# Optimization experiments

Measured on AMD Instinct MI355X. Metric: run time of the kernel, lower is better.

Reference implementation:

```python
import jax, jax.numpy as jnp
import numpy as np

SEQ_LEN = 12  # configs['seq_len']
B, N, E = 4, 50000, 1600000
F_IN, F_OUT = 12, 48


def setup_inputs() -> dict:
    key = jax.random.key(0)
    k_x, k_ei, k_ew, k_w = jax.random.split(key, 4)
    x = jax.random.normal(k_x, (B, N, F_IN), dtype=jnp.float32)
    edge_index = jax.random.randint(k_ei, (B, 2, E), 0, N, dtype=jnp.int32)
    edge_attr = jax.random.uniform(k_ew, (B, E), dtype=jnp.float32)  # positive edge weights
    W = jax.random.normal(k_w, (F_IN, F_OUT), dtype=jnp.float32) * (1.0 / np.sqrt(F_IN))
    b = jnp.zeros((F_OUT,), dtype=jnp.float32)
    return {"x": x, "edge_index": edge_index, "edge_attr": edge_attr, "W": W, "b": b}


def _gcn_conv(x, src, dst, ew, W, b):
    # PyG GCNConv with edge_weight: A_hat = D^-1/2 (A + I) D^-1/2, x' = A_hat x W + b
    n = x.shape[0]
    xw = x @ W                                            # [N, F_OUT]
    deg = jax.ops.segment_sum(ew, dst, num_segments=n) + 1.0  # +1 for self loop weight
    dinv = jax.lax.rsqrt(deg)                             # deg > 0 guaranteed by self loops
    norm = dinv[src] * ew * dinv[dst]                     # [E]
    msg = xw[src] * norm[:, None]                         # [E, F_OUT] gathered messages
    agg = jax.ops.segment_sum(msg, dst, num_segments=n)   # scatter-add to destinations
    agg = agg + xw * (dinv * dinv)[:, None]               # self-loop contribution (weight 1)
    return agg + b


def reference(x, edge_index, edge_attr, W, b):
    def one_graph(xg, eig, ewg):
        h = _gcn_conv(xg, eig[0], eig[1], ewg, W, b)      # [N, F_OUT]
        # dropout is identity in eval mode
        h = h.reshape(h.shape[0], SEQ_LEN, -1)            # [N, seq_len, d]
        return jnp.transpose(h, (1, 0, 2))                # [seq_len, N, d]

    return jax.vmap(one_graph)(x, edge_index, edge_attr)  # stacked: [B, seq_len, N, d]
```

## Files before the change

kernel.cpp:

```cpp
#include <hip/hip_runtime.h>

#define BATCH 4
#define NNODE 50000
#define NEDGE 1600000
#define F_IN 12
#define F_OUT 48
#define SEQ 12

#define BNODE 64
#define NBUCK ((NNODE + BNODE - 1) / BNODE)
#define NBINS (BATCH * NBUCK)
#define SCAN_N 4096
#define EBLK 4096
#define EPB_C (EBLK / 256)
#define EPB_F (EBLK / 512)
#define NFB ((NEDGE + EBLK - 1) / EBLK)
#define CAPB 2560
#define MAXR (CAPB / 256)

typedef float f4v __attribute__((ext_vector_type(4)));


__global__ void __launch_bounds__(256) k_zero(int* __restrict__ cnt) {
    int i = blockIdx.x * 256 + threadIdx.x;
    if (i < SCAN_N) cnt[i] = 0;
}

__global__ void __launch_bounds__(256) k_count(const int* __restrict__ ei,
                                               int* __restrict__ cnt) {
    __shared__ int h[NBUCK];
    int t = threadIdx.x;
    for (int i = t; i < NBUCK; i += 256) h[i] = 0;
    __syncthreads();
    int b = blockIdx.y;
    int e0 = blockIdx.x * EBLK;
    const int* dsts = ei + ((size_t)b * 2 + 1) * NEDGE;
    for (int it = 0; it < EPB_C; ++it) {
        int e = e0 + it * 256 + t;
        if (e < NEDGE) atomicAdd(&h[dsts[e] >> 6], 1);
    }
    __syncthreads();
    for (int i = t; i < NBUCK; i += 256) {
        int c = h[i];
        if (c) atomicAdd(&cnt[b * NBUCK + i], c);
    }
}

__global__ void __launch_bounds__(256) k_scan(const int* __restrict__ cnt,
                                              int* __restrict__ off,
                                              int* __restrict__ cur) {
    __shared__ int w[256];
    int t = threadIdx.x;
    int base = t * 16;
    int loc[16];
    int s = 0;
#pragma unroll
    for (int j = 0; j < 16; j++) { loc[j] = cnt[base + j]; s += loc[j]; }
    w[t] = s;
    __syncthreads();
    for (int d = 1; d < 256; d <<= 1) {
        int v = (t >= d) ? w[t - d] : 0;
        __syncthreads();
        w[t] += v;
        __syncthreads();
    }
    int run = w[t] - s;
#pragma unroll
    for (int j = 0; j < 16; j++) {
        int i = base + j;
        off[i] = run;
        if (i < NBINS) cur[i] = run;
        run += loc[j];
    }
}

__global__ void __launch_bounds__(512) k_fill(const int* __restrict__ ei,
                                              const float* __restrict__ ew,
                                              int* __restrict__ cur,
                                              int2* __restrict__ rec) {
    __shared__ int h[1024];
    __shared__ int loff[1024];
    __shared__ int gbase[NBUCK];
    __shared__ int2 srec[EBLK];
    __shared__ int w[512];

    int t = threadIdx.x;
    int b = blockIdx.y;
    int e0 = blockIdx.x * EBLK;
    for (int i = t; i < 1024; i += 512) h[i] = 0;
    __syncthreads();

    const size_t ebase = (size_t)b * 2 * NEDGE;
    const int* srcs = ei + ebase;
    const int* dsts = ei + ebase + NEDGE;
    const float* ws = ew + (size_t)b * NEDGE;

    int2 myrec[EPB_F];
    int mypk[EPB_F];
#pragma unroll
    for (int it = 0; it < EPB_F; ++it) {
        int e = e0 + it * 512 + t;
        int valid = e < NEDGE;
        int src = 0, dst = 0;
        float wv = 0.0f;
        if (valid) { src = srcs[e]; dst = dsts[e]; wv = ws[e]; }
        int g = dst >> 6;
        int r = 0;
        if (valid) r = atomicAdd(&h[g], 1);
        myrec[it] = make_int2((dst << 16) | src, __float_as_int(wv));
        mypk[it] = valid ? ((g << 16) | r) : -1;
    }
    __syncthreads();

    int c0 = h[2 * t], c1 = h[2 * t + 1];
    int ls = c0 + c1;
    w[t] = ls;
    __syncthreads();
    for (int d = 1; d < 512; d <<= 1) {
        int v = (t >= d) ? w[t - d] : 0;
        __syncthreads();
        w[t] += v;
        __syncthreads();
    }
    int excl = w[t] - ls;
    loff[2 * t] = excl;
    loff[2 * t + 1] = excl + c0;
    __syncthreads();

    for (int i = t; i < NBUCK; i += 512) {
        int c = h[i];
        if (c) gbase[i] = atomicAdd(&cur[b * NBUCK + i], c);
    }
#pragma unroll
    for (int it = 0; it < EPB_F; ++it) {
        int pk = mypk[it];
        if (pk >= 0) {
            int g = pk >> 16, r = pk & 0xFFFF;
            srec[loff[g] + r] = myrec[it];
        }
    }
    __syncthreads();

    int nvalid = min(EBLK, NEDGE - e0);
    for (int j = t; j < nvalid; j += 512) {
        int2 rv = srec[j];
        int g = ((unsigned)rv.x) >> 22;
        rec[gbase[g] + (j - loff[g])] = rv;
    }
}


__global__ void __launch_bounds__(256) k_sortdeg(const int* __restrict__ off,
                                                 int2* rec,
                                                 const float* __restrict__ x,
                                                 float* __restrict__ dinv,
                                                 float* __restrict__ xs,
                                                 int* __restrict__ nodebase) {
    __shared__ int2 srec[CAPB];
    __shared__ int hh[BNODE];
    __shared__ int basev[BNODE];
    __shared__ int wsc[BNODE];

    int t = threadIdx.x;
    int bid = blockIdx.x;
    int xcd = bid & 7;
    int b = xcd >> 1;
    int gl = ((bid >> 3) << 1) + (xcd & 1);
    int bin = b * NBUCK + gl;

    if (t < BNODE) hh[t] = 0;
    __syncthreads();

    int s = off[bin], e = off[bin + 1];
    const unsigned long long* rp = (const unsigned long long*)rec;

    int2 myrec[MAXR];
    int mypk[MAXR];
#pragma unroll
    for (int i = 0; i < MAXR; i++) {
        mypk[i] = -1;
        int j = s + i * 256 + t;
        if (j < e) {
            unsigned long long rv = rp[j];
            int key = (int)(rv & 0xFFFFFFFFull);
            myrec[i] = make_int2(key, (int)(rv >> 32));
            int node = (key >> 16) & 63;
            int r = atomicAdd(&hh[node], 1);
            mypk[i] = (r << 6) | node;
        }
    }
    __syncthreads();

    if (t < BNODE) wsc[t] = hh[t];
    __syncthreads();
    for (int d = 1; d < BNODE; d <<= 1) {
        int v = 0;
        if (t < BNODE && t >= d) v = wsc[t - d];
        __syncthreads();
        if (t < BNODE) wsc[t] += v;
        __syncthreads();
    }
    if (t < BNODE) basev[t] = wsc[t] - hh[t];
    __syncthreads();

#pragma unroll
    for (int i = 0; i < MAXR; i++) {
        int pk = mypk[i];
        if (pk >= 0) srec[basev[pk & 63] + (pk >> 6)] = myrec[i];
    }
    __syncthreads();

    int cntr = e - s;
    for (int j = t; j < cntr; j += 256) rec[s + j] = srec[j];
    if (t < BNODE) nodebase[bin * BNODE + t] = s + basev[t];

    int node = t >> 2, par = t & 3;
    int rs = basev[node], cn = hh[node];
    float sum = 0.0f;
    for (int j = rs + par; j < rs + cn; j += 4)
        sum += __int_as_float(srec[j].y);
    sum += __shfl_xor(sum, 1);
    sum += __shfl_xor(sum, 2);
    float rsq = rsqrtf(1.0f + sum);

    int n = gl * BNODE + node;
    if (n >= NNODE) return;
    size_t gi = (size_t)b * NNODE + n;
    if (par == 0) dinv[gi] = rsq;
    f4v o = {0.f, 0.f, 0.f, 0.f};
    if (par < 3) {
        const f4v* x4 = (const f4v*)(x + gi * F_IN);
        f4v v = x4[par];
        o.x = rsq * v.x; o.y = rsq * v.y; o.z = rsq * v.z; o.w = rsq * v.w;
    }
    ((f4v*)xs)[gi * 4 + par] = o;
}

__global__ void __launch_bounds__(256) k_gather2(const int* __restrict__ off,
                                                 const int2* __restrict__ rec,
                                                 const int* __restrict__ nodebase,
                                                 const float* __restrict__ xs,
                                                 const float* __restrict__ dinv,
                                                 const float* __restrict__ Wm,
                                                 const float* __restrict__ bias,
                                                 float* __restrict__ out) {
    __shared__ float sW[F_IN * F_OUT];
    __shared__ float sb[F_OUT];
    __shared__ int nb[BNODE + 1];

    int t = threadIdx.x;
    int bid = blockIdx.x;
    int xcd = bid & 7;
    int b = xcd >> 1;
    int gl = ((bid >> 3) << 1) + (xcd & 1);
    int bin = b * NBUCK + gl;

    for (int i = t; i < F_IN * F_OUT; i += 256) sW[i] = Wm[i];
    if (t < F_OUT) sb[t] = bias[t];
    if (t < BNODE) nb[t] = nodebase[bin * BNODE + t];
    if (t == 0) nb[BNODE] = off[bin + 1];
    __syncthreads();

    int node = t >> 2, par = t & 3;
    int rs = nb[node], re = nb[node + 1];
    const f4v* xs4 = (const f4v*)xs + (size_t)b * NNODE * 4;
    const unsigned long long* rp = (const unsigned long long*)rec;

    float a[F_IN];
#pragma unroll
    for (int k = 0; k < F_IN; k++) a[k] = 0.0f;
    for (int j = rs + par; j < re; j += 4) {
        unsigned long long rv = rp[j];
        int key = (int)(rv & 0xFFFFFFFFull);
        float wv = __int_as_float((int)(rv >> 32));
        const f4v* xp = xs4 + (size_t)(key & 0xFFFF) * 4;
        f4v v0 = xp[0], v1 = xp[1], v2 = xp[2];
        a[0] += wv * v0.x;  a[1] += wv * v0.y;  a[2]  += wv * v0.z;  a[3]  += wv * v0.w;
        a[4] += wv * v1.x;  a[5] += wv * v1.y;  a[6]  += wv * v1.z;  a[7]  += wv * v1.w;
        a[8] += wv * v2.x;  a[9] += wv * v2.y;  a[10] += wv * v2.z;  a[11] += wv * v2.w;
    }
#pragma unroll
    for (int k = 0; k < F_IN; k++) {
        a[k] += __shfl_xor(a[k], 1);
        a[k] += __shfl_xor(a[k], 2);
    }

    int n = gl * BNODE + node;
    if (n >= NNODE) return;
    float di = dinv[(size_t)b * NNODE + n];
    const f4v* xn = xs4 + (size_t)n * 4;
    f4v s0 = xn[0], s1 = xn[1], s2 = xn[2];
    float xsn[F_IN] = {s0.x, s0.y, s0.z, s0.w, s1.x, s1.y, s1.z, s1.w,
                       s2.x, s2.y, s2.z, s2.w};
#pragma unroll
    for (int k = 0; k < F_IN; k++) a[k] = di * (a[k] + xsn[k]);

    float hv[12];
#pragma unroll
    for (int j = 0; j < 12; j++) {
        int jj = par * 12 + j;
        float v = sb[jj];
#pragma unroll
        for (int k = 0; k < F_IN; k++) v = fmaf(a[k], sW[k * F_OUT + jj], v);
        hv[j] = v;
    }
    f4v* out4 = (f4v*)out;
#pragma unroll
    for (int q = 0; q < 3; q++) {
        int sq = par * 3 + q;
        f4v v = {hv[q * 4 + 0], hv[q * 4 + 1], hv[q * 4 + 2], hv[q * 4 + 3]};
        __builtin_nontemporal_store(v, out4 + (size_t)(b * SEQ + sq) * NNODE + n);
    }
}

extern "C" void kernel_launch(void* const* d_in, const int* in_sizes, int n_in,
                              void* d_out, int out_size, void* d_ws, size_t ws_size,
                              hipStream_t stream) {
    const float* x  = (const float*)d_in[0];
    const int*   ei = (const int*)d_in[1];
    const float* ew = (const float*)d_in[2];
    const float* Wm = (const float*)d_in[3];
    const float* bv = (const float*)d_in[4];
    float* out = (float*)d_out;

    int2*  rec = (int2*)d_ws;
    float* xs  = (float*)(rec + (size_t)BATCH * NEDGE);
    int*   cnt = (int*)(xs + (size_t)BATCH * NNODE * 16);
    int*   off = cnt + SCAN_N;
    int*   cur = off + SCAN_N;
    float* dinv = (float*)(cur + NBINS);
    int*   nodebase = (int*)(dinv + (size_t)BATCH * NNODE);

    k_zero<<<SCAN_N / 256, 256, 0, stream>>>(cnt);
    {
        dim3 grid(NFB, BATCH);
        k_count<<<grid, 256, 0, stream>>>(ei, cnt);
    }
    k_scan<<<1, 256, 0, stream>>>(cnt, off, cur);
    {
        dim3 grid(NFB, BATCH);
        k_fill<<<grid, 512, 0, stream>>>(ei, ew, cur, rec);
    }
    k_sortdeg<<<8 * (NBUCK / 2), 256, 0, stream>>>(off, rec, x, dinv, xs, nodebase);
    k_gather2<<<8 * (NBUCK / 2), 256, 0, stream>>>(off, rec, nodebase, xs, dinv, Wm, bv, out);
}
```

Before: 291.4 us.

## Split gather across lanes by feature chunk instead of by edge

The four lanes assigned to a node now each load one 16-byte feature chunk of every incoming edge, rather than each lane loading all three chunks for a strided subset of edges. This makes the per-edge feature loads coalesced across the quad and replaces the 12-value xor-shuffle reduction with 12 broadcast shuffles. Record loads become nontemporal and the edge loop is unrolled by two. The cost is that every lane walks the full edge list, so record loads are repeated per lane, the fourth lane sits idle during the gather, and the dependent chain per lane is longer.

```diff
diff --git a/kernel.cpp b/kernel.cpp
--- a/kernel.cpp
+++ b/kernel.cpp
@@ -266,43 +266,55 @@
     const f4v* xs4 = (const f4v*)xs + (size_t)b * NNODE * 4;
     const unsigned long long* rp = (const unsigned long long*)rec;
 
+    f4v acc = {0.f, 0.f, 0.f, 0.f};
+    int j = rs;
+    for (; j + 2 <= re; j += 2) {
+        unsigned long long rv0 = __builtin_nontemporal_load(rp + j);
+        unsigned long long rv1 = __builtin_nontemporal_load(rp + j + 1);
+        if (par < 3) {
+            int k0 = (int)(rv0 & 0xFFFFFFFFull);
+            int k1 = (int)(rv1 & 0xFFFFFFFFull);
+            float w0 = __int_as_float((int)(rv0 >> 32));
+            float w1 = __int_as_float((int)(rv1 >> 32));
+            f4v v0 = xs4[(size_t)(k0 & 0xFFFF) * 4 + par];
+            f4v v1 = xs4[(size_t)(k1 & 0xFFFF) * 4 + par];
+            acc += w0 * v0;
+            acc += w1 * v1;
+        }
+    }
+    if (j < re) {
+        unsigned long long rv0 = __builtin_nontemporal_load(rp + j);
+        if (par < 3) {
+            int k0 = (int)(rv0 & 0xFFFFFFFFull);
+            float w0 = __int_as_float((int)(rv0 >> 32));
+            acc += w0 * xs4[(size_t)(k0 & 0xFFFF) * 4 + par];
+        }
+    }
+
+    int n = gl * BNODE + node;
+    float di = (n < NNODE) ? dinv[(size_t)b * NNODE + n] : 0.0f;
+    if (n < NNODE && par < 3) acc += xs4[(size_t)n * 4 + par];
+    acc *= di;
+
+    int base = t & ~3;
     float a[F_IN];
 #pragma unroll
-    for (int k = 0; k < F_IN; k++) a[k] = 0.0f;
-    for (int j = rs + par; j < re; j += 4) {
-        unsigned long long rv = rp[j];
-        int key = (int)(rv & 0xFFFFFFFFull);
-        float wv = __int_as_float((int)(rv >> 32));
-        const f4v* xp = xs4 + (size_t)(key & 0xFFFF) * 4;
-        f4v v0 = xp[0], v1 = xp[1], v2 = xp[2];
-        a[0] += wv * v0.x;  a[1] += wv * v0.y;  a[2]  += wv * v0.z;  a[3]  += wv * v0.w;
-        a[4] += wv * v1.x;  a[5] += wv * v1.y;  a[6]  += wv * v1.z;  a[7]  += wv * v1.w;
-        a[8] += wv * v2.x;  a[9] += wv * v2.y;  a[10] += wv * v2.z;  a[11] += wv * v2.w;
-    }
-#pragma unroll
-    for (int k = 0; k < F_IN; k++) {
-        a[k] += __shfl_xor(a[k], 1);
-        a[k] += __shfl_xor(a[k], 2);
-    }
-
-    int n = gl * BNODE + node;
+    for (int k = 0; k < 3; k++) {
+        a[4 * k + 0] = __shfl(acc.x, base + k);
+        a[4 * k + 1] = __shfl(acc.y, base + k);
+        a[4 * k + 2] = __shfl(acc.z, base + k);
+        a[4 * k + 3] = __shfl(acc.w, base + k);
+    }
+
     if (n >= NNODE) return;
-    float di = dinv[(size_t)b * NNODE + n];
-    const f4v* xn = xs4 + (size_t)n * 4;
-    f4v s0 = xn[0], s1 = xn[1], s2 = xn[2];
-    float xsn[F_IN] = {s0.x, s0.y, s0.z, s0.w, s1.x, s1.y, s1.z, s1.w,
-                       s2.x, s2.y, s2.z, s2.w};
-#pragma unroll
-    for (int k = 0; k < F_IN; k++) a[k] = di * (a[k] + xsn[k]);
-
     float hv[12];
 #pragma unroll
-    for (int j = 0; j < 12; j++) {
-        int jj = par * 12 + j;
+    for (int jo = 0; jo < 12; jo++) {
+        int jj = par * 12 + jo;
         float v = sb[jj];
 #pragma unroll
         for (int k = 0; k < F_IN; k++) v = fmaf(a[k], sW[k * F_OUT + jj], v);
-        hv[j] = v;
+        hv[jo] = v;
     }
     f4v* out4 = (f4v*)out;
 #pragma unroll
```

Measured after the change: 331.6 us. 13.8% more time.
